# Performance work log

Hardware: AMD Instinct MI355X
Metric: run time of the kernel (lower is better)

Reference implementation:

```python
import jax, jax.numpy as jnp
import numpy as np

B_COEF = 0.1          # position-offset scale 'b'
STRIDE = (1, 1)
PADDING = (1, 1)


def setup_inputs() -> dict:
    key = jax.random.key(0)
    k1, k2, k3 = jax.random.split(key, 3)
    x = jax.random.normal(k1, (16, 64, 128, 128), dtype=jnp.float32)
    kernel = jax.random.normal(k2, (128, 64, 3, 3), dtype=jnp.float32)
    bias = jax.random.normal(k3, (128,), dtype=jnp.float32)
    return {"x": x, "kernel": kernel, "bias": bias}


def _conv(inp, w):
    pads = [(PADDING[0], PADDING[0]), (PADDING[1], PADDING[1])]
    return jax.lax.conv_general_dilated(
        inp, w, window_strides=STRIDE, padding=pads,
        dimension_numbers=("NCHW", "OIHW", "NCHW"))


def reference(x, kernel, bias):
    # out[b,o,p] = sum_i x_unf[b,i,p] * (kernel_flat[o,i] + b*grid[p]) + bias[o]
    # = conv(x, kernel) + b*grid[p] * sum_i x_unf[b,i,p] + bias  (rank-1 separable)
    kh, kw = kernel.shape[2], kernel.shape[3]
    main = _conv(x, kernel)                                  # (B, O, Ho, Wo)
    H_out, W_out = main.shape[2], main.shape[3]

    # sum over in_channels and kernel window = ones-conv of channel-summed input
    ones_k = jnp.ones((1, 1, kh, kw), dtype=x.dtype)
    patch_sum = _conv(x.sum(axis=1, keepdims=True), ones_k)  # (B, 1, Ho, Wo)

    # Replicate torch meshgrid(arange(W_out), arange(H_out), indexing='ij')
    # -> flatten (W,H) row-major -> consumed as (H,W) row-major by the view.
    gx = jnp.arange(W_out)[:, None] + jnp.arange(H_out)[None, :]  # (Wo, Ho)
    grid2d = gx.reshape(-1).reshape(H_out, W_out).astype(x.dtype)  # (Ho, Wo)

    return main + B_COEF * grid2d * patch_sum + bias[None, :, None, None]
```

## Files before the change

kernel.cpp:

```cpp
#include <hip/hip_runtime.h>
#include <hip/hip_bf16.h>


typedef __attribute__((ext_vector_type(8))) short short8;
typedef __attribute__((ext_vector_type(4))) float f32x4;

#define B_COEF 0.1f
constexpr int CI = 64, CO = 128, H = 128, W = 128;
constexpr int XPAD = 72;

static __device__ inline short bf16s(float v) {
    __hip_bfloat16 b = __float2bfloat16(v);
    return *reinterpret_cast<short*>(&b);
}


__global__ void prep_wq(const float* __restrict__ wgt, __hip_bfloat16* __restrict__ wq) {
    int idx = blockIdx.x * 256 + threadIdx.x;
    if (idx < 9 * CO * CI) {
        int tap = idx >> 13;
        int rem = idx & 8191;
        int oc = rem >> 6, ci = rem & 63;
        int kc = ci >> 5, j = ci & 31;
        wq[(((tap * 2 + kc) * CO + oc) << 5) + j] =
            __float2bfloat16(wgt[(oc * CI + ci) * 9 + tap]);
    }
}

__global__ __launch_bounds__(256, 3)
void conv_fused(const float* __restrict__ x,
                const __hip_bfloat16* __restrict__ wq,
                const float* __restrict__ bias,
                float* __restrict__ out) {
    __shared__ __hip_bfloat16 xrow[3][130 * 64];
    __shared__ float psum[256];
    __shared__ float ssumL[130];

    const int tid = threadIdx.x, bx = blockIdx.x, b = blockIdx.y;
    const int h = ((bx & 7) << 4) | (bx >> 3);
    const int lane = tid & 63, waveid = tid >> 6;
    const int lo16 = lane & 15, quad = lane >> 4;
    const int m0 = (waveid & 1) * 64, n0 = (waveid >> 1) * 64;

    if (tid < 48) {
        const int r = tid >> 4, s = ((tid >> 3) & 1) ? 129 : 0, u = tid & 7;
        short8 z = {0, 0, 0, 0, 0, 0, 0, 0};
        *(short8*)&xrow[r][s * 64 + ((u ^ (s & 7)) * 8)] = z;
    }

    const int wl = tid & 127, cg0 = tid >> 7;
    const int wslot = wl + 1, wsw = wslot & 7;
    float sacc = 0.0f;
    const float* xb = x + (size_t)b * CI * H * W + wl;
#pragma unroll
    for (int p = 0; p < 4; ++p) {
        const int cg = cg0 + 2 * p;
#pragma unroll
        for (int r = 0; r < 3; ++r) {
            const int gh = h - 1 + r;
            short8 pk = {0, 0, 0, 0, 0, 0, 0, 0};
            if (gh >= 0 && gh < H) {
                const float* px = xb + ((size_t)(cg * 8) * H + gh) * W;
                float v[8];
#pragma unroll
                for (int j = 0; j < 8; ++j) v[j] = px[(size_t)j * H * W];
#pragma unroll
                for (int j = 0; j < 8; ++j) {
                    pk[j] = bf16s(v[j]);
                    sacc += v[j];
                }
            }
            *(short8*)&xrow[r][wslot * 64 + ((cg ^ wsw) * 8)] = pk;
        }
    }
    psum[tid] = sacc;
    __syncthreads();

    if (tid < 128) ssumL[tid + 1] = psum[tid] + psum[tid + 128];
    if (tid == 128) ssumL[0] = 0.0f;
    if (tid == 129) ssumL[129] = 0.0f;
    __syncthreads();

    f32x4 acc[4][4] = {};

    __builtin_amdgcn_s_setprio(1);
#pragma unroll
    for (int kh = 0; kh < 3; ++kh) {
#pragma unroll
        for (int kw = 0; kw < 3; ++kw) {
            const int tap = kh * 3 + kw;
            short8 bq[2][4];
#pragma unroll
            for (int kc = 0; kc < 2; ++kc)
#pragma unroll
                for (int ni = 0; ni < 4; ++ni)
                    bq[kc][ni] = *(const short8*)(
                        wq + (((tap * 2 + kc) * CO + n0 + ni * 16 + lo16) << 5) + quad * 8);
#pragma unroll
            for (int kc = 0; kc < 2; ++kc) {
                short8 af[4];
#pragma unroll
                for (int mi = 0; mi < 4; ++mi) {
                    const int row = m0 + mi * 16 + lo16 + kw;
                    af[mi] = *(const short8*)
                        &xrow[kh][row * 64 + (((kc * 4 + quad) ^ (row & 7)) * 8)];
                }
#pragma unroll
                for (int mi = 0; mi < 4; ++mi)
#pragma unroll
                    for (int ni = 0; ni < 4; ++ni)
                        acc[mi][ni] = __builtin_amdgcn_mfma_f32_16x16x32_bf16(
                            af[mi], bq[kc][ni], acc[mi][ni], 0, 0, 0);
            }
        }
    }
    __builtin_amdgcn_s_setprio(0);

#pragma unroll
    for (int mi = 0; mi < 4; ++mi) {
        const int wbase = m0 + mi * 16 + quad * 4;
        float cs[6];
#pragma unroll
        for (int t = 0; t < 6; ++t) cs[t] = ssumL[wbase + t];
        float ps[4], cf[4];
#pragma unroll
        for (int t = 0; t < 4; ++t) {
            ps[t] = cs[t] + cs[t + 1] + cs[t + 2];
            cf[t] = B_COEF * (float)(h + wbase + t);
        }
#pragma unroll
        for (int ni = 0; ni < 4; ++ni) {
            const int oc = n0 + ni * 16 + lo16;
            const float bv = bias[oc];
            f32x4 v = acc[mi][ni];
#pragma unroll
            for (int t = 0; t < 4; ++t) v[t] = v[t] + cf[t] * ps[t] + bv;
            *(f32x4*)(out + (((size_t)b * CO + oc) * H + h) * W + wbase) = v;
        }
    }
}


constexpr int WPAD = 72;

__global__ void prep_w_fb(const float* __restrict__ wgt, __hip_bfloat16* __restrict__ wt) {
    int idx = blockIdx.x * 256 + threadIdx.x;
    if (idx < 9 * CO * CI) {
        int tap = idx / (CO * CI);
        int rem = idx - tap * (CO * CI);
        int oc = rem >> 6, ci = rem & 63;
        wt[idx] = __float2bfloat16(wgt[(oc * CI + ci) * 9 + tap]);
    }
}

__global__ __launch_bounds__(256, 2)
void conv_fb(const float* __restrict__ x, const __hip_bfloat16* __restrict__ wt,
             const float* __restrict__ bias, float* __restrict__ out) {
    __shared__ __hip_bfloat16 xrow[130 * XPAD];
    __shared__ __hip_bfloat16 wlds[CO * WPAD];
    __shared__ float colsum[132];

    const int tid = threadIdx.x;
    const int h = blockIdx.x, b = blockIdx.y;
    const int lane = tid & 63, waveid = tid >> 6;
    const int lo16 = lane & 15, quad = lane >> 4;
    const int m0 = (waveid & 1) * 64, n0 = (waveid >> 1) * 64;

    f32x4 acc[4][4] = {};
    if (tid < 132) colsum[tid] = 0.0f;
    const float* xb = x + (size_t)b * CI * H * W;

    const int w16 = tid & 15, cipl = (tid >> 4) & 3, rest0 = tid >> 6;

    for (int kh = 0; kh < 3; ++kh) {
        const int gh = h - 1 + kh;
        __syncthreads();
        for (int it = 0; it < 18; ++it) {
            int rest = rest0 + it * 4;
            int whi = rest % 9, ciph = rest / 9;
            int w = whi * 16 + w16;
            int ci0 = (ciph * 4 + cipl) * 2;
            int gw = w - 1;
            float x0 = 0.0f, x1 = 0.0f;
            if (w < 130 && gw >= 0 && gw < W && gh >= 0 && gh < H) {
                const float* p = xb + (size_t)ci0 * (H * W) + gh * W + gw;
                x0 = p[0];
                x1 = p[H * W];
            }
            if (w < 130) {
                __hip_bfloat162 pk;
                pk.x = __float2bfloat16(x0);
                pk.y = __float2bfloat16(x1);
                *(__hip_bfloat162*)&xrow[w * XPAD + ci0] = pk;
            }
            float cs = x0 + x1;
            cs += __shfl_xor(cs, 16);
            cs += __shfl_xor(cs, 32);
            if (quad == 0 && w < 130) atomicAdd(&colsum[w], cs);
        }
        for (int kw = 0; kw < 3; ++kw) {
            __syncthreads();
            {
                const __hip_bfloat16* wtap = wt + (kh * 3 + kw) * (CO * CI);
#pragma unroll
                for (int it = 0; it < 4; ++it) {
                    int j = tid + it * 256;
                    int oc = j >> 3, ch = (j & 7) * 8;
                    short8 v = *(const short8*)(wtap + oc * CI + ch);
                    *(short8*)&wlds[oc * WPAD + ch] = v;
                }
            }
            __syncthreads();
#pragma unroll
            for (int kc = 0; kc < 2; ++kc) {
                const int krow = kc * 32 + quad * 8;
                short8 af[4], bf[4];
#pragma unroll
                for (int mi = 0; mi < 4; ++mi)
                    af[mi] = *(const short8*)&xrow[(m0 + mi * 16 + lo16 + kw) * XPAD + krow];
#pragma unroll
                for (int ni = 0; ni < 4; ++ni)
                    bf[ni] = *(const short8*)&wlds[(n0 + ni * 16 + lo16) * WPAD + krow];
#pragma unroll
                for (int mi = 0; mi < 4; ++mi)
#pragma unroll
                    for (int ni = 0; ni < 4; ++ni)
                        acc[mi][ni] = __builtin_amdgcn_mfma_f32_16x16x32_bf16(
                            af[mi], bf[ni], acc[mi][ni], 0, 0, 0);
            }
        }
    }
    __syncthreads();
#pragma unroll
    for (int mi = 0; mi < 4; ++mi) {
        const int wbase = m0 + mi * 16 + quad * 4;
        float cs[6];
#pragma unroll
        for (int r = 0; r < 6; ++r) cs[r] = colsum[wbase + r];
        float ps[4], cf[4];
#pragma unroll
        for (int r = 0; r < 4; ++r) {
            ps[r] = cs[r] + cs[r + 1] + cs[r + 2];
            cf[r] = B_COEF * (float)(h + wbase + r);
        }
#pragma unroll
        for (int ni = 0; ni < 4; ++ni) {
            const int oc = n0 + ni * 16 + lo16;
            const float bv = bias[oc];
            f32x4 v = acc[mi][ni];
#pragma unroll
            for (int r = 0; r < 4; ++r) v[r] = v[r] + cf[r] * ps[r] + bv;
            *(f32x4*)(out + (((size_t)b * CO + oc) * H + h) * W + wbase) = v;
        }
    }
}


extern "C" void kernel_launch(void* const* d_in, const int* in_sizes, int n_in,
                              void* d_out, int out_size, void* d_ws, size_t ws_size,
                              hipStream_t stream) {
    const float* x    = (const float*)d_in[0];
    const float* wgt  = (const float*)d_in[1];
    const float* bias = (const float*)d_in[2];
    float* out = (float*)d_out;

    const size_t WQ_BYTES = (size_t)9 * 2 * CO * 32 * 2;

    if (ws_size >= WQ_BYTES) {
        __hip_bfloat16* wq = (__hip_bfloat16*)d_ws;
        prep_wq<<<dim3(288), dim3(256), 0, stream>>>(wgt, wq);
        conv_fused<<<dim3(H, 16), dim3(256), 0, stream>>>(x, wq, bias, out);
    } else {
        __hip_bfloat16* wt = (__hip_bfloat16*)d_ws;
        prep_w_fb<<<dim3(288), dim3(256), 0, stream>>>(wgt, wt);
        conv_fb<<<dim3(H, 16), dim3(256), 0, stream>>>(x, wt, bias, out);
    }
}
```

Measured before the change: 229.9 us.

## Process four output rows per block with rolling row buffer and prefetch

Each block now computes SH=4 consecutive output rows, keeping a 3-row rolling bf16 LDS ring so each input row is loaded once per block instead of three times. The next input row is prefetched into registers while the MFMA work for the current row runs, then written to LDS after a barrier. Column sums are kept per row and combined for the patch-sum term. This cuts global input traffic and hides load latency, but it launches a quarter as many blocks, lowers occupancy to 2 blocks per CU, and adds more barriers.

```diff
diff --git a/kernel.cpp b/kernel.cpp
--- a/kernel.cpp
+++ b/kernel.cpp
@@ -7,11 +7,23 @@
 
 #define B_COEF 0.1f
 constexpr int CI = 64, CO = 128, H = 128, W = 128;
+constexpr int SH = 4;
 constexpr int XPAD = 72;
 
 static __device__ inline short bf16s(float v) {
     __hip_bfloat16 b = __float2bfloat16(v);
     return *reinterpret_cast<short*>(&b);
+}
+
+static __device__ inline void bar_lgkm() {
+    asm volatile("s_waitcnt lgkmcnt(0)" ::: "memory");
+    __builtin_amdgcn_s_barrier();
+    asm volatile("" ::: "memory");
+}
+static __device__ inline void bar_plain() {
+    asm volatile("" ::: "memory");
+    __builtin_amdgcn_s_barrier();
+    asm volatile("" ::: "memory");
 }
 
 
@@ -27,115 +39,162 @@
     }
 }
 
-__global__ __launch_bounds__(256, 3)
+static __device__ __forceinline__ void loadrow(const float* __restrict__ xb, int r,
+                                               int wl, int cg0, float* pf) {
+    if ((unsigned)r < (unsigned)H) {
+        const float* px = xb + (size_t)r * W + wl;
+#pragma unroll
+        for (int p = 0; p < 4; ++p) {
+            const int cg = cg0 + 2 * p;
+#pragma unroll
+            for (int j = 0; j < 8; ++j)
+                pf[p * 8 + j] = px[(size_t)(cg * 8 + j) * (H * W)];
+        }
+    } else {
+#pragma unroll
+        for (int i = 0; i < 32; ++i) pf[i] = 0.0f;
+    }
+}
+
+static __device__ __forceinline__ void writerow(__hip_bfloat16* __restrict__ xs,
+                                                float* __restrict__ psb, int tid,
+                                                int wslot, int cg0, const float* pf) {
+    const int wsw = wslot & 7;
+    float part = 0.0f;
+#pragma unroll
+    for (int p = 0; p < 4; ++p) {
+        const int cg = cg0 + 2 * p;
+        short8 pk;
+#pragma unroll
+        for (int j = 0; j < 8; ++j) {
+            pk[j] = bf16s(pf[p * 8 + j]);
+            part += pf[p * 8 + j];
+        }
+        *(short8*)&xs[wslot * 64 + ((cg ^ wsw) * 8)] = pk;
+    }
+    psb[tid] = part;
+}
+
+__global__ __launch_bounds__(256, 2)
 void conv_fused(const float* __restrict__ x,
                 const __hip_bfloat16* __restrict__ wq,
                 const float* __restrict__ bias,
                 float* __restrict__ out) {
     __shared__ __hip_bfloat16 xrow[3][130 * 64];
-    __shared__ float psum[256];
-    __shared__ float ssumL[130];
+    __shared__ float Srow[3][132];
+    __shared__ float ps3[132];
+    __shared__ float psb[256];
 
     const int tid = threadIdx.x, bx = blockIdx.x, b = blockIdx.y;
-    const int h = ((bx & 7) << 4) | (bx >> 3);
+    const int u = ((bx & 7) << 2) | (bx >> 3);
+    const int h0 = u * SH;
     const int lane = tid & 63, waveid = tid >> 6;
     const int lo16 = lane & 15, quad = lane >> 4;
     const int m0 = (waveid & 1) * 64, n0 = (waveid >> 1) * 64;
+    const int wl = tid & 127, cg0 = tid >> 7, wslot = wl + 1;
+
+    const float* xb = x + (size_t)b * CI * H * W;
 
     if (tid < 48) {
-        const int r = tid >> 4, s = ((tid >> 3) & 1) ? 129 : 0, u = tid & 7;
+        const int sl = tid >> 4, col = (tid & 8) ? 129 : 0, uu = tid & 7;
         short8 z = {0, 0, 0, 0, 0, 0, 0, 0};
-        *(short8*)&xrow[r][s * 64 + ((u ^ (s & 7)) * 8)] = z;
-    }
-
-    const int wl = tid & 127, cg0 = tid >> 7;
-    const int wslot = wl + 1, wsw = wslot & 7;
-    float sacc = 0.0f;
-    const float* xb = x + (size_t)b * CI * H * W + wl;
-#pragma unroll
-    for (int p = 0; p < 4; ++p) {
-        const int cg = cg0 + 2 * p;
-#pragma unroll
-        for (int r = 0; r < 3; ++r) {
-            const int gh = h - 1 + r;
-            short8 pk = {0, 0, 0, 0, 0, 0, 0, 0};
-            if (gh >= 0 && gh < H) {
-                const float* px = xb + ((size_t)(cg * 8) * H + gh) * W;
-                float v[8];
-#pragma unroll
-                for (int j = 0; j < 8; ++j) v[j] = px[(size_t)j * H * W];
-#pragma unroll
-                for (int j = 0; j < 8; ++j) {
-                    pk[j] = bf16s(v[j]);
-                    sacc += v[j];
+        *(short8*)&xrow[sl][col * 64 + ((uu ^ (col & 7)) * 8)] = z;
+    }
+    if (tid == 48) ps3[0] = 0.0f;
+    if (tid == 49) ps3[129] = 0.0f;
+
+#pragma unroll
+    for (int k = 0; k < 2; ++k) {
+        const int r = h0 - 1 + k;
+        float pf[32];
+        loadrow(xb, r, wl, cg0, pf);
+        writerow(&xrow[(r + 1) % 3][0], psb, tid, wslot, cg0, pf);
+        bar_lgkm();
+        if (tid < 128) Srow[(r + 1) % 3][tid + 1] = psb[tid] + psb[tid + 128];
+        bar_lgkm();
+    }
+    {
+        float pf[32];
+        loadrow(xb, h0 + 1, wl, cg0, pf);
+        writerow(&xrow[(h0 + 2) % 3][0], psb, tid, wslot, cg0, pf);
+        bar_lgkm();
+    }
+
+    for (int t = 0; t < SH; ++t) {
+        const int h = h0 + t;
+
+        float pf[32];
+        if (t < SH - 1) loadrow(xb, h + 2, wl, cg0, pf);
+
+        if (tid < 128) {
+            const float v = psb[tid] + psb[tid + 128];
+            Srow[(h + 2) % 3][tid + 1] = v;
+            ps3[tid + 1] = Srow[h % 3][tid + 1] + Srow[(h + 1) % 3][tid + 1] + v;
+        }
+        bar_lgkm();
+
+        f32x4 acc[4][4] = {};
+        __builtin_amdgcn_s_setprio(1);
+#pragma unroll
+        for (int kh = 0; kh < 3; ++kh) {
+            const __hip_bfloat16* xs = &xrow[(h + kh) % 3][0];
+#pragma unroll
+            for (int kw = 0; kw < 3; ++kw) {
+                const int tap = kh * 3 + kw;
+                short8 bq[2][4];
+#pragma unroll
+                for (int kc = 0; kc < 2; ++kc)
+#pragma unroll
+                    for (int ni = 0; ni < 4; ++ni)
+                        bq[kc][ni] = *(const short8*)(
+                            wq + (((tap * 2 + kc) * CO + n0 + ni * 16 + lo16) << 5) + quad * 8);
+#pragma unroll
+                for (int kc = 0; kc < 2; ++kc) {
+                    short8 af[4];
+#pragma unroll
+                    for (int mi = 0; mi < 4; ++mi) {
+                        const int row = m0 + mi * 16 + lo16 + kw;
+                        af[mi] = *(const short8*)
+                            &xs[row * 64 + (((kc * 4 + quad) ^ (row & 7)) * 8)];
+                    }
+#pragma unroll
+                    for (int mi = 0; mi < 4; ++mi)
+#pragma unroll
+                        for (int ni = 0; ni < 4; ++ni)
+                            acc[mi][ni] = __builtin_amdgcn_mfma_f32_16x16x32_bf16(
+                                af[mi], bq[kc][ni], acc[mi][ni], 0, 0, 0);
                 }
             }
-            *(short8*)&xrow[r][wslot * 64 + ((cg ^ wsw) * 8)] = pk;
-        }
-    }
-    psum[tid] = sacc;
-    __syncthreads();
-
-    if (tid < 128) ssumL[tid + 1] = psum[tid] + psum[tid + 128];
-    if (tid == 128) ssumL[0] = 0.0f;
-    if (tid == 129) ssumL[129] = 0.0f;
-    __syncthreads();
-
-    f32x4 acc[4][4] = {};
-
-    __builtin_amdgcn_s_setprio(1);
-#pragma unroll
-    for (int kh = 0; kh < 3; ++kh) {
-#pragma unroll
-        for (int kw = 0; kw < 3; ++kw) {
-            const int tap = kh * 3 + kw;
-            short8 bq[2][4];
-#pragma unroll
-            for (int kc = 0; kc < 2; ++kc)
-#pragma unroll
-                for (int ni = 0; ni < 4; ++ni)
-                    bq[kc][ni] = *(const short8*)(
-                        wq + (((tap * 2 + kc) * CO + n0 + ni * 16 + lo16) << 5) + quad * 8);
-#pragma unroll
-            for (int kc = 0; kc < 2; ++kc) {
-                short8 af[4];
-#pragma unroll
-                for (int mi = 0; mi < 4; ++mi) {
-                    const int row = m0 + mi * 16 + lo16 + kw;
-                    af[mi] = *(const short8*)
-                        &xrow[kh][row * 64 + (((kc * 4 + quad) ^ (row & 7)) * 8)];
-                }
-#pragma unroll
-                for (int mi = 0; mi < 4; ++mi)
-#pragma unroll
-                    for (int ni = 0; ni < 4; ++ni)
-                        acc[mi][ni] = __builtin_amdgcn_mfma_f32_16x16x32_bf16(
-                            af[mi], bq[kc][ni], acc[mi][ni], 0, 0, 0);
-            }
-        }
-    }
-    __builtin_amdgcn_s_setprio(0);
-
-#pragma unroll
-    for (int mi = 0; mi < 4; ++mi) {
-        const int wbase = m0 + mi * 16 + quad * 4;
-        float cs[6];
-#pragma unroll
-        for (int t = 0; t < 6; ++t) cs[t] = ssumL[wbase + t];
-        float ps[4], cf[4];
-#pragma unroll
-        for (int t = 0; t < 4; ++t) {
-            ps[t] = cs[t] + cs[t + 1] + cs[t + 2];
-            cf[t] = B_COEF * (float)(h + wbase + t);
-        }
-#pragma unroll
-        for (int ni = 0; ni < 4; ++ni) {
-            const int oc = n0 + ni * 16 + lo16;
-            const float bv = bias[oc];
-            f32x4 v = acc[mi][ni];
-#pragma unroll
-            for (int t = 0; t < 4; ++t) v[t] = v[t] + cf[t] * ps[t] + bv;
-            *(f32x4*)(out + (((size_t)b * CO + oc) * H + h) * W + wbase) = v;
+        }
+        __builtin_amdgcn_s_setprio(0);
+
+#pragma unroll
+        for (int mi = 0; mi < 4; ++mi) {
+            const int wbase = m0 + mi * 16 + quad * 4;
+            float cs[6];
+#pragma unroll
+            for (int q2 = 0; q2 < 6; ++q2) cs[q2] = ps3[wbase + q2];
+            float ps[4], cf[4];
+#pragma unroll
+            for (int q2 = 0; q2 < 4; ++q2) {
+                ps[q2] = cs[q2] + cs[q2 + 1] + cs[q2 + 2];
+                cf[q2] = B_COEF * (float)(h + wbase + q2);
+            }
+#pragma unroll
+            for (int ni = 0; ni < 4; ++ni) {
+                const int oc = n0 + ni * 16 + lo16;
+                const float bv = bias[oc];
+                f32x4 v = acc[mi][ni];
+#pragma unroll
+                for (int q2 = 0; q2 < 4; ++q2) v[q2] = v[q2] + cf[q2] * ps[q2] + bv;
+                *(f32x4*)(out + (((size_t)b * CO + oc) * H + h) * W + wbase) = v;
+            }
+        }
+        bar_plain();
+
+        if (t < SH - 1) {
+            writerow(&xrow[h % 3][0], psb, tid, wslot, cg0, pf);
+            bar_lgkm();
         }
     }
 }
@@ -269,7 +328,7 @@
     if (ws_size >= WQ_BYTES) {
         __hip_bfloat16* wq = (__hip_bfloat16*)d_ws;
         prep_wq<<<dim3(288), dim3(256), 0, stream>>>(wgt, wq);
-        conv_fused<<<dim3(H, 16), dim3(256), 0, stream>>>(x, wq, bias, out);
+        conv_fused<<<dim3(H / SH, 16), dim3(256), 0, stream>>>(x, wq, bias, out);
     } else {
         __hip_bfloat16* wt = (__hip_bfloat16*)d_ws;
         prep_w_fb<<<dim3(288), dim3(256), 0, stream>>>(wgt, wt);
```

New measurement: 258.2 us. 1.12x slower.

## Split each output row into two 64-column half-row tiles with halo loading

Applied to the files above, without the earlier changes.

Each block now computes half an output row (64 columns) instead of a full row, doubling the grid to 2*H x 16. The halo columns are loaded and channel-summed separately with a wave-level shuffle reduction. Shared memory per block shrinks and the occupancy hint rises from 3 to 5 blocks per CU, aiming at more latency hiding. In exchange, each wave does half the MFMA work per weight load and halo reads add some redundant global traffic.

```diff
diff --git a/kernel.cpp b/kernel.cpp
--- a/kernel.cpp
+++ b/kernel.cpp
@@ -12,6 +12,12 @@
 static __device__ inline short bf16s(float v) {
     __hip_bfloat16 b = __float2bfloat16(v);
     return *reinterpret_cast<short*>(&b);
+}
+
+static __device__ inline void bar_lgkm() {
+    asm volatile("s_waitcnt lgkmcnt(0)" ::: "memory");
+    __builtin_amdgcn_s_barrier();
+    asm volatile("" ::: "memory");
 }
 
 
@@ -27,65 +33,89 @@
     }
 }
 
-__global__ __launch_bounds__(256, 3)
+__global__ __launch_bounds__(256, 5)
 void conv_fused(const float* __restrict__ x,
                 const __hip_bfloat16* __restrict__ wq,
                 const float* __restrict__ bias,
                 float* __restrict__ out) {
-    __shared__ __hip_bfloat16 xrow[3][130 * 64];
+    __shared__ __hip_bfloat16 xrow[3][66 * 64];
     __shared__ float psum[256];
-    __shared__ float ssumL[130];
+    __shared__ float ssumL[66];
+    __shared__ float Shalo[8];
 
     const int tid = threadIdx.x, bx = blockIdx.x, b = blockIdx.y;
-    const int h = ((bx & 7) << 4) | (bx >> 3);
+    const int u = ((bx & 7) << 5) | (bx >> 3);
+    const int h = u >> 1, w0 = (u & 1) * 64;
     const int lane = tid & 63, waveid = tid >> 6;
     const int lo16 = lane & 15, quad = lane >> 4;
-    const int m0 = (waveid & 1) * 64, n0 = (waveid >> 1) * 64;
-
-    if (tid < 48) {
-        const int r = tid >> 4, s = ((tid >> 3) & 1) ? 129 : 0, u = tid & 7;
-        short8 z = {0, 0, 0, 0, 0, 0, 0, 0};
-        *(short8*)&xrow[r][s * 64 + ((u ^ (s & 7)) * 8)] = z;
-    }
-
-    const int wl = tid & 127, cg0 = tid >> 7;
-    const int wslot = wl + 1, wsw = wslot & 7;
+    const int m0 = (waveid & 1) * 32;
+    const int n0 = (waveid >> 1) * 64;
+
+    const float* xb = x + (size_t)b * CI * H * W;
+
+    const int c = tid & 63, cu = tid >> 6;
+    const int slot = c + 1, ssw = slot & 7;
     float sacc = 0.0f;
-    const float* xb = x + (size_t)b * CI * H * W + wl;
-#pragma unroll
-    for (int p = 0; p < 4; ++p) {
-        const int cg = cg0 + 2 * p;
-#pragma unroll
-        for (int r = 0; r < 3; ++r) {
-            const int gh = h - 1 + r;
-            short8 pk = {0, 0, 0, 0, 0, 0, 0, 0};
-            if (gh >= 0 && gh < H) {
-                const float* px = xb + ((size_t)(cg * 8) * H + gh) * W;
-                float v[8];
-#pragma unroll
-                for (int j = 0; j < 8; ++j) v[j] = px[(size_t)j * H * W];
-#pragma unroll
-                for (int j = 0; j < 8; ++j) {
-                    pk[j] = bf16s(v[j]);
-                    sacc += v[j];
-                }
-            }
-            *(short8*)&xrow[r][wslot * 64 + ((cg ^ wsw) * 8)] = pk;
+#pragma unroll
+    for (int r = 0; r < 3; ++r) {
+        const int gh = h - 1 + r;
+        float v[16];
+        if ((unsigned)gh < (unsigned)H) {
+            const float* px = xb + ((size_t)(cu * 16) * H + gh) * W + w0 + c;
+#pragma unroll
+            for (int j = 0; j < 16; ++j) v[j] = px[(size_t)j * H * W];
+        } else {
+#pragma unroll
+            for (int j = 0; j < 16; ++j) v[j] = 0.0f;
+        }
+#pragma unroll
+        for (int hf = 0; hf < 2; ++hf) {
+            short8 pk;
+#pragma unroll
+            for (int j = 0; j < 8; ++j) {
+                pk[j] = bf16s(v[hf * 8 + j]);
+                sacc += v[hf * 8 + j];
+            }
+            const int unit = cu * 2 + hf;
+            *(short8*)&xrow[r][slot * 64 + ((unit ^ ssw) * 8)] = pk;
         }
     }
     psum[tid] = sacc;
-    __syncthreads();
-
-    if (tid < 128) ssumL[tid + 1] = psum[tid] + psum[tid + 128];
-    if (tid == 128) ssumL[0] = 0.0f;
-    if (tid == 129) ssumL[129] = 0.0f;
-    __syncthreads();
-
-    f32x4 acc[4][4] = {};
-
+
+#pragma unroll
+    for (int it = 0; it < 2; ++it) {
+        const int f = it * 256 + tid;
+        if (f < 384) {
+            const int wv = f >> 6, ci = f & 63;
+            const int r = wv >> 1, hc = wv & 1;
+            const int gh = h - 1 + r, gw = hc ? (w0 + 64) : (w0 - 1);
+            float val = 0.0f;
+            if ((unsigned)gh < (unsigned)H && (unsigned)gw < (unsigned)W)
+                val = xb[((size_t)ci * H + gh) * W + gw];
+            const int hs = hc ? 65 : 0;
+            xrow[r][hs * 64 + (((ci >> 3) ^ (hs & 7)) * 8) + (ci & 7)] =
+                __float2bfloat16(val);
+            float s = val;
+#pragma unroll
+            for (int off = 1; off < 64; off <<= 1) s += __shfl_xor(s, off);
+            if (ci == 0) Shalo[wv] = s;
+        }
+    }
+    bar_lgkm();
+
+    if (tid < 64)
+        ssumL[tid + 1] = psum[tid] + psum[tid + 64] + psum[tid + 128] + psum[tid + 192];
+    else if (tid == 64)
+        ssumL[0] = Shalo[0] + Shalo[2] + Shalo[4];
+    else if (tid == 65)
+        ssumL[65] = Shalo[1] + Shalo[3] + Shalo[5];
+    bar_lgkm();
+
+    f32x4 acc[2][4] = {};
     __builtin_amdgcn_s_setprio(1);
 #pragma unroll
     for (int kh = 0; kh < 3; ++kh) {
+        const __hip_bfloat16* xs = &xrow[kh][0];
 #pragma unroll
         for (int kw = 0; kw < 3; ++kw) {
             const int tap = kh * 3 + kw;
@@ -98,15 +128,15 @@
                         wq + (((tap * 2 + kc) * CO + n0 + ni * 16 + lo16) << 5) + quad * 8);
 #pragma unroll
             for (int kc = 0; kc < 2; ++kc) {
-                short8 af[4];
-#pragma unroll
-                for (int mi = 0; mi < 4; ++mi) {
-                    const int row = m0 + mi * 16 + lo16 + kw;
+                short8 af[2];
+#pragma unroll
+                for (int mi = 0; mi < 2; ++mi) {
+                    const int sl = m0 + mi * 16 + lo16 + kw;
                     af[mi] = *(const short8*)
-                        &xrow[kh][row * 64 + (((kc * 4 + quad) ^ (row & 7)) * 8)];
+                        &xs[sl * 64 + (((kc * 4 + quad) ^ (sl & 7)) * 8)];
                 }
 #pragma unroll
-                for (int mi = 0; mi < 4; ++mi)
+                for (int mi = 0; mi < 2; ++mi)
 #pragma unroll
                     for (int ni = 0; ni < 4; ++ni)
                         acc[mi][ni] = __builtin_amdgcn_mfma_f32_16x16x32_bf16(
@@ -117,7 +147,7 @@
     __builtin_amdgcn_s_setprio(0);
 
 #pragma unroll
-    for (int mi = 0; mi < 4; ++mi) {
+    for (int mi = 0; mi < 2; ++mi) {
         const int wbase = m0 + mi * 16 + quad * 4;
         float cs[6];
 #pragma unroll
@@ -126,7 +156,7 @@
 #pragma unroll
         for (int t = 0; t < 4; ++t) {
             ps[t] = cs[t] + cs[t + 1] + cs[t + 2];
-            cf[t] = B_COEF * (float)(h + wbase + t);
+            cf[t] = B_COEF * (float)(h + w0 + wbase + t);
         }
 #pragma unroll
         for (int ni = 0; ni < 4; ++ni) {
@@ -135,7 +165,7 @@
             f32x4 v = acc[mi][ni];
 #pragma unroll
             for (int t = 0; t < 4; ++t) v[t] = v[t] + cf[t] * ps[t] + bv;
-            *(f32x4*)(out + (((size_t)b * CO + oc) * H + h) * W + wbase) = v;
+            *(f32x4*)(out + (((size_t)b * CO + oc) * H + h) * W + w0 + wbase) = v;
         }
     }
 }
@@ -269,7 +299,7 @@
     if (ws_size >= WQ_BYTES) {
         __hip_bfloat16* wq = (__hip_bfloat16*)d_ws;
         prep_wq<<<dim3(288), dim3(256), 0, stream>>>(wgt, wq);
-        conv_fused<<<dim3(H, 16), dim3(256), 0, stream>>>(x, wq, bias, out);
+        conv_fused<<<dim3(2 * H, 16), dim3(256), 0, stream>>>(x, wq, bias, out);
     } else {
         __hip_bfloat16* wt = (__hip_bfloat16*)d_ws;
         prep_w_fb<<<dim3(288), dim3(256), 0, stream>>>(wgt, wt);
```

Result: slower. 254.0 us (+10.5%).
